# Performance work log

Measured on AMD Instinct MI355X. Metric: run time of the kernel, lower is better.

Reference implementation:

```python
import jax, jax.numpy as jnp
import numpy as np

N, T = 32, 1500
ENC_DIM, DEC_DIM = 1024, 1024
ATT_DIM, ATT_HEAD = 512, 4
HA = ATT_DIM * ATT_HEAD


def setup_inputs() -> dict:
    key = jax.random.key(0)
    ks = jax.random.split(key, 12)
    enc_pad = jax.random.normal(ks[0], (N, T, ENC_DIM), dtype=jnp.float32)
    enc_len = jax.random.randint(ks[1], (N,), T // 2, T + 1)
    enc_len = enc_len.at[0].set(T)  # ensure max == T (original code assumes mask width == T)
    dec_prev = jax.random.normal(ks[2], (N, DEC_DIM), dtype=jnp.float32)
    ali_prev = jnp.zeros((N, T), dtype=jnp.float32)  # unused by forward
    s = 0.02
    W_enc = jax.random.normal(ks[3], (ENC_DIM, HA), dtype=jnp.float32) * s
    b_enc = jnp.zeros((HA,), dtype=jnp.float32)
    W_key = jax.random.normal(ks[4], (ENC_DIM, HA), dtype=jnp.float32) * s
    W_dec = jax.random.normal(ks[5], (DEC_DIM, HA), dtype=jnp.float32) * s
    W_ctx = jax.random.normal(ks[6], (HA, ENC_DIM), dtype=jnp.float32) * s
    b_ctx = jnp.zeros((ENC_DIM,), dtype=jnp.float32)
    # grouped Conv1d(HA -> H, kernel=1, groups=H, bias=False): weight [H, A]
    w_conv = jax.random.normal(ks[7], (ATT_HEAD, ATT_DIM), dtype=jnp.float32) * s
    return dict(enc_pad=enc_pad, enc_len=enc_len, dec_prev=dec_prev, ali_prev=ali_prev,
                W_enc=W_enc, b_enc=b_enc, W_key=W_key, W_dec=W_dec,
                W_ctx=W_ctx, b_ctx=b_ctx, w_conv=w_conv)


def reference(enc_pad, enc_len, dec_prev, ali_prev,
              W_enc, b_enc, W_key, W_dec, W_ctx, b_ctx, w_conv):
    n, t, _ = enc_pad.shape
    H, A = ATT_HEAD, ATT_DIM
    # enc_part: N x H x T x A
    enc_part = (enc_pad @ W_enc + b_enc).reshape(n, t, H, A).transpose(0, 2, 1, 3)
    # key_part: N x H x A x T
    key_part = (enc_pad @ W_key).reshape(n, t, H, A).transpose(0, 2, 3, 1)
    # dec_part: N x H x A
    dec_part = (dec_prev @ W_dec).reshape(n, H, A)
    # additive score: tanh(key + dec), grouped 1x1 conv scorer -> N x H x T
    sum_part = jnp.tanh(key_part + dec_part[:, :, :, None])
    e = jnp.einsum('nhat,ha->nht', sum_part, w_conv)
    # padding mask: True where t >= enc_len
    pad_mask = jnp.arange(t)[None, :] >= enc_len[:, None]  # N x T
    e = jnp.where(pad_mask[:, None, :], -jnp.inf, e)
    ali = jax.nn.softmax(e, axis=-1)  # N x H x T
    # weighted sum over time, then context projection
    ctx = jnp.einsum('nht,nhta->nha', ali, enc_part).reshape(n, H * A)
    ctx = ctx @ W_ctx + b_ctx  # N x D_enc
    return ali, ctx
```

## Files before the change

### kernel.cpp

```cpp
#include <hip/hip_runtime.h>
#include <hip/hip_bf16.h>


#define N_B   32
#define T_S   1500
#define ENC_D 1024
#define HA_D  2048
#define A_D   512
#define H_N   4
#define MROWS 48000

typedef short s8v  __attribute__((ext_vector_type(8)));
typedef float f32x4 __attribute__((ext_vector_type(4)));

__device__ __forceinline__ unsigned short f2bf(float f) {
    unsigned u = __float_as_uint(f);
    unsigned r = (u + 0x7FFFu + ((u >> 16) & 1u)) >> 16;
    return (unsigned short)r;
}
__device__ __forceinline__ float bf2f(unsigned short b) {
    return __uint_as_float(((unsigned)b) << 16);
}
__device__ __forceinline__ float fast_tanh(float x) {
    float e2 = __expf(2.0f * x);
    return 1.0f - __fdividef(2.0f, e2 + 1.0f);
}
__device__ __forceinline__ void gload_lds16(const void* g, void* l) {
    __builtin_amdgcn_global_load_lds(
        (const unsigned int __attribute__((address_space(1)))*)g,
        (unsigned int __attribute__((address_space(3)))*)l, 16, 0, 0);
}

__device__ __forceinline__ void skinny_body(
    int bid, const float* __restrict__ X, const float* __restrict__ W,
    const float* __restrict__ bias, float* __restrict__ Y,
    int Ncols, int ct_mask, int ct_shift, int xA, int xB, float* xT ) {
    const int tid = threadIdx.x;
    const int ct = bid & ct_mask, ks = bid >> ct_shift;
    const int c0 = ct << 8, k0 = ks << 6;
    const int hsel = c0 >> 9;
    {
        const int n = tid >> 3, kk0 = (tid & 7) << 3;
        const float* xr = X + (size_t)n * xA + hsel * xB + k0 + kk0;
        float4 v0 = *(const float4*)xr;
        float4 v1 = *(const float4*)(xr + 4);
        xT[(kk0 + 0) * 36 + n] = v0.x;
        xT[(kk0 + 1) * 36 + n] = v0.y;
        xT[(kk0 + 2) * 36 + n] = v0.z;
        xT[(kk0 + 3) * 36 + n] = v0.w;
        xT[(kk0 + 4) * 36 + n] = v1.x;
        xT[(kk0 + 5) * 36 + n] = v1.y;
        xT[(kk0 + 6) * 36 + n] = v1.z;
        xT[(kk0 + 7) * 36 + n] = v1.w;
    }
    __syncthreads();
    const int w = tid >> 6, lane = tid & 63;
    f32x4 acc[8];
    if (bias != nullptr && ks == 0) {
        f32x4 bv = *(const f32x4*)&bias[c0 + (lane << 2)];
#pragma unroll
        for (int j = 0; j < 8; ++j) acc[j] = bv;
    } else {
#pragma unroll
        for (int j = 0; j < 8; ++j) { f32x4 z = {0.f, 0.f, 0.f, 0.f}; acc[j] = z; }
    }
    const float* Wp = W + (size_t)k0 * Ncols + c0 + (lane << 2);
#pragma unroll 4
    for (int kk = 0; kk < 64; ++kk) {
        f32x4 wf = *(const f32x4*)(Wp + (size_t)kk * Ncols);
        f32x4 xlo = *(const f32x4*)&xT[kk * 36 + w * 8];
        f32x4 xhi = *(const f32x4*)&xT[kk * 36 + w * 8 + 4];
#pragma unroll
        for (int j = 0; j < 4; ++j) {
            acc[j]     += xlo[j] * wf;
            acc[4 + j] += xhi[j] * wf;
        }
    }
#pragma unroll
    for (int j = 0; j < 8; ++j) {
        float* yp = Y + (size_t)(w * 8 + j) * Ncols + c0 + (lane << 2);
#pragma unroll
        for (int i = 0; i < 4; ++i) atomicAdd(yp + i, acc[j][i]);
    }
}

__global__ __launch_bounds__(256) void skinny_k(
    const float* __restrict__ X, const float* __restrict__ W,
    const float* __restrict__ bias, float* __restrict__ Y,
    int Ncols, int ct_mask, int ct_shift, int xA, int xB) {
    __shared__ float xT[64 * 36];
    skinny_body(blockIdx.x, X, W, bias, Y, Ncols, ct_mask, ct_shift, xA, xB, xT);
}

__global__ __launch_bounds__(256) void prep_k(
    const float* __restrict__ enc_pad, const float* __restrict__ Wk,
    const float* __restrict__ dec_prev, const float* __restrict__ W_dec,
    unsigned short* __restrict__ Xb, unsigned short* __restrict__ Wt,
    float* __restrict__ dp) {
    __shared__ float shmem[64 * 65];
    const int b = blockIdx.x;
    const int tid = threadIdx.x;
    if (b < 128) {
        skinny_body(b, dec_prev, W_dec, nullptr, dp, HA_D, 7, 3, 1024, 0, shmem);
    } else if (b < 640) {
        float (*ld)[65] = (float(*)[65])shmem;
        const int bb = b - 128;
        const int tx = tid & 63, ty = tid >> 6;
        const int c0 = (bb & 31) * 64, d0 = (bb >> 5) * 64;
#pragma unroll
        for (int j = 0; j < 16; ++j)
            ld[ty + 4 * j][tx] = Wk[(size_t)(d0 + ty + 4 * j) * HA_D + c0 + tx];
        __syncthreads();
#pragma unroll
        for (int j = 0; j < 16; ++j)
            Wt[(size_t)(c0 + ty + 4 * j) * ENC_D + d0 + tx] = f2bf(ld[tx][ty + 4 * j]);
    } else {
        const float4* in = (const float4*)enc_pad;
        ushort4* out = (ushort4*)Xb;
        for (int i = (b - 640) * 256 + tid; i < 12288000; i += 3000 * 256) {
            float4 v = in[i];
            ushort4 o;
            o.x = f2bf(v.x); o.y = f2bf(v.y); o.z = f2bf(v.z); o.w = f2bf(v.w);
            out[i] = o;
        }
    }
}

__global__ __launch_bounds__(512) void fused_score_k(
    const unsigned short* __restrict__ Xb, const unsigned short* __restrict__ Wt,
    const float* __restrict__ dec, const float* __restrict__ wconv,
    const int* __restrict__ enc_len, float* __restrict__ e_out) {
    __shared__ unsigned short As[128 * 64];
    __shared__ unsigned short Bs[256 * 64];
    __shared__ float e_s[128];

    const int tid = threadIdx.x;
    const int lane = tid & 63, wid = tid >> 6;
    const int wr = wid >> 2, wc = wid & 3;
    const int l15 = lane & 15, lhi = lane >> 4;

    int orig = blockIdx.x;
    int wgid = (orig & 7) * 375 + (orig >> 3);
    const int mtile = wgid >> 3, nt = wgid & 7;
    const int r0 = mtile * 128;
    const int bcol0 = nt * 256;
    const int h = nt >> 1;

    {
        int n0 = (int)((unsigned)r0 / 1500u);
        int t0 = r0 - n0 * 1500;
        if (t0 + 127 < 1500 && t0 >= enc_len[n0]) return;
    }

    if (tid < 128) e_s[tid] = 0.f;

    const unsigned short* aSrc[2]; int aDst[2];
#pragma unroll
    for (int ld = 0; ld < 2; ++ld) {
        int li = ld * 512 + tid, rowL = li >> 3, c16 = li & 7;
        aSrc[ld] = Xb + (size_t)(r0 + rowL) * ENC_D + ((c16 ^ (rowL & 7)) << 3);
        aDst[ld] = li * 8;
    }
    const unsigned short* bSrc[4]; int bDst[4];
#pragma unroll
    for (int ld = 0; ld < 4; ++ld) {
        int li = ld * 512 + tid, colL = li >> 3, c16 = li & 7;
        bSrc[ld] = Wt + (size_t)(bcol0 + colL) * ENC_D + ((c16 ^ (colL & 7)) << 3);
        bDst[ld] = li * 8;
    }

    const int cA0 = (lhi * 8) ^ ((l15 & 7) << 3);
    const int cA1 = (32 + lhi * 8) ^ ((l15 & 7) << 3);
    const int arow = wr * 64 + l15;
    const int bcol = wc * 64 + l15;

    f32x4 acc[4][4];
#pragma unroll
    for (int m = 0; m < 4; ++m)
#pragma unroll
        for (int n2 = 0; n2 < 4; ++n2) {
            f32x4 z = {0.f, 0.f, 0.f, 0.f};
            acc[m][n2] = z;
        }

    for (int ks = 0; ks < 16; ++ks) {
        const int kb = ks << 6;
#pragma unroll
        for (int ld = 0; ld < 2; ++ld) gload_lds16(aSrc[ld] + kb, As + aDst[ld]);
#pragma unroll
        for (int ld = 0; ld < 4; ++ld) gload_lds16(bSrc[ld] + kb, Bs + bDst[ld]);
        __syncthreads();
#pragma unroll
        for (int kk = 0; kk < 2; ++kk) {
            const int cc = kk ? cA1 : cA0;
            s8v af[4], bv[4];
#pragma unroll
            for (int m = 0; m < 4; ++m)
                af[m] = *(const s8v*)&As[(arow + m * 16) * 64 + cc];
#pragma unroll
            for (int n2 = 0; n2 < 4; ++n2)
                bv[n2] = *(const s8v*)&Bs[(bcol + n2 * 16) * 64 + cc];
#pragma unroll
            for (int m = 0; m < 4; ++m)
#pragma unroll
                for (int n2 = 0; n2 < 4; ++n2)
                    acc[m][n2] = __builtin_amdgcn_mfma_f32_16x16x32_bf16(af[m], bv[n2], acc[m][n2], 0, 0, 0);
        }
        __syncthreads();
    }

    float wv[4];
#pragma unroll
    for (int n2 = 0; n2 < 4; ++n2)
        wv[n2] = wconv[bcol0 + wc * 64 + n2 * 16 + l15];
#pragma unroll
    for (int m = 0; m < 4; ++m) {
#pragma unroll
        for (int rg = 0; rg < 4; ++rg) {
            int row_l = wr * 64 + m * 16 + lhi * 4 + rg;
            int grow = r0 + row_l;
            int nn = (int)((unsigned)grow / 1500u);
            const float* dsl = dec + (size_t)nn * HA_D + bcol0 + wc * 64 + l15;
            float s = 0.f;
#pragma unroll
            for (int n2 = 0; n2 < 4; ++n2) {
                float v = acc[m][n2][rg] + dsl[n2 * 16];
                s += wv[n2] * fast_tanh(v);
            }
            s += __shfl_xor(s, 1); s += __shfl_xor(s, 2);
            s += __shfl_xor(s, 4); s += __shfl_xor(s, 8);
            if (l15 == 0) atomicAdd(&e_s[row_l], s);
        }
    }
    __syncthreads();
    if (tid < 128) {
        int grow = r0 + tid;
        int nn = grow / 1500, tt = grow - nn * 1500;
        atomicAdd(&e_out[(size_t)(nn * H_N + h) * T_S + tt], e_s[tid]);
    }
}

__global__ void softmax_k(const float* __restrict__ e, const int* __restrict__ enc_len,
                          float* __restrict__ ali, float* __restrict__ ctx_zero) {
    const int tid = threadIdx.x, lane = tid & 63, wid = tid >> 6;
    ctx_zero[blockIdx.x * 256 + tid] = 0.f;
    const int n = blockIdx.x >> 2;
    const int len = enc_len[n];
    const float* row = e + (size_t)blockIdx.x * T_S;
    float* orow = ali + (size_t)blockIdx.x * T_S;
    __shared__ float red[4];
    float p[6];
    float mx = -__builtin_inff();
#pragma unroll
    for (int i = 0; i < 6; ++i) {
        int t = tid + i * 256;
        float v = -__builtin_inff();
        if (t < T_S && t < len) v = row[t];
        p[i] = v;
        mx = fmaxf(mx, v);
    }
#pragma unroll
    for (int o = 32; o; o >>= 1) mx = fmaxf(mx, __shfl_xor(mx, o));
    if (lane == 0) red[wid] = mx;
    __syncthreads();
    mx = fmaxf(fmaxf(red[0], red[1]), fmaxf(red[2], red[3]));
    __syncthreads();
    float sum = 0.f;
#pragma unroll
    for (int i = 0; i < 6; ++i) {
        float qv = (p[i] == -__builtin_inff()) ? 0.f : __expf(p[i] - mx);
        p[i] = qv;
        sum += qv;
    }
#pragma unroll
    for (int o = 32; o; o >>= 1) sum += __shfl_xor(sum, o);
    if (lane == 0) red[wid] = sum;
    __syncthreads();
    sum = red[0] + red[1] + red[2] + red[3];
    float inv = 1.0f / sum;
#pragma unroll
    for (int i = 0; i < 6; ++i) {
        int t = tid + i * 256;
        if (t < T_S) orow[t] = p[i] * inv;
    }
}

__global__ __launch_bounds__(256) void wenc_k(const unsigned short* __restrict__ Xb,
                                              const float* __restrict__ ali,
                                              const int* __restrict__ enc_len,
                                              float* __restrict__ wenc) {
    const int tid = threadIdx.x;
    const int n = blockIdx.x & 31, tq = blockIdx.x >> 5;
    const int t0 = tq * 94;
    const int tcnt = (t0 + 94 <= T_S) ? 94 : (T_S - t0);
    if (t0 >= enc_len[n]) return;
    __shared__ float alis[4][94];
    for (int i = tid; i < 376; i += 256) {
        int hh = i / 94, tt = i - hh * 94;
        if (tt < tcnt) alis[hh][tt] = ali[(size_t)(n * H_N + hh) * T_S + t0 + tt];
    }
    __syncthreads();
    const int d0 = tid * 4;
    float a[4][4] = {};
    const unsigned short* xp = Xb + (size_t)(n * T_S + t0) * ENC_D + d0;
#pragma unroll 4
    for (int t = 0; t < tcnt; ++t) {
        ushort4 xv = *(const ushort4*)&xp[(size_t)t * ENC_D];
        float x0 = bf2f(xv.x), x1 = bf2f(xv.y), x2 = bf2f(xv.z), x3 = bf2f(xv.w);
#pragma unroll
        for (int hh = 0; hh < 4; ++hh) {
            float al = alis[hh][t];
            a[hh][0] = fmaf(al, x0, a[hh][0]);
            a[hh][1] = fmaf(al, x1, a[hh][1]);
            a[hh][2] = fmaf(al, x2, a[hh][2]);
            a[hh][3] = fmaf(al, x3, a[hh][3]);
        }
    }
#pragma unroll
    for (int hh = 0; hh < 4; ++hh)
#pragma unroll
        for (int j = 0; j < 4; ++j)
            atomicAdd(&wenc[(size_t)(n * H_N + hh) * ENC_D + d0 + j], a[hh][j]);
}

extern "C" void kernel_launch(void* const* d_in, const int* in_sizes, int n_in,
                              void* d_out, int out_size, void* d_ws, size_t ws_size,
                              hipStream_t stream) {
    const float* enc_pad  = (const float*)d_in[0];
    const int*   enc_len  = (const int*)d_in[1];
    const float* dec_prev = (const float*)d_in[2];
    const float* W_enc    = (const float*)d_in[4];
    const float* b_enc    = (const float*)d_in[5];
    const float* W_key    = (const float*)d_in[6];
    const float* W_dec    = (const float*)d_in[7];
    const float* W_ctx    = (const float*)d_in[8];
    const float* b_ctx    = (const float*)d_in[9];
    const float* w_conv   = (const float*)d_in[10];

    char* ws = (char*)d_ws;
    unsigned short* Xb = (unsigned short*)ws;
    unsigned short* Wt = (unsigned short*)(ws + 98304000);
    float* dp   = (float*)(ws + 102498304);
    float* e    = (float*)(ws + 102760448);
    float* wenc = (float*)(ws + 103528448);
    float* cpre = (float*)(ws + 104052736);

    float* ali = (float*)d_out;
    float* ctx = ((float*)d_out) + 192000;

    hipMemsetAsync(ws + 102498304, 0, 1816576, stream);
    prep_k<<<3640, 256, 0, stream>>>(enc_pad, W_key, dec_prev, W_dec, Xb, Wt, dp);
    fused_score_k<<<3000, 512, 0, stream>>>(Xb, Wt, dp, w_conv, enc_len, e);
    softmax_k<<<128, 256, 0, stream>>>(e, enc_len, ali, ctx);
    wenc_k<<<512, 256, 0, stream>>>(Xb, ali, enc_len, wenc);
    skinny_k<<<128, 256, 0, stream>>>(wenc, W_enc, b_enc, cpre, HA_D, 7, 3, 4096, 1024);
    skinny_k<<<128, 256, 0, stream>>>(cpre, W_ctx, b_ctx, ctx, ENC_D, 3, 2, 2048, 0);
}
```

Measured before the change: 405.5 us.

## Fuse softmax into weighted-sum kernel and skip bf16 conversion of padded rows

The enc_pad-to-bf16 conversion in prep_k is now tiled per (batch, 16-timestep chunk) and skips chunks beyond enc_len, so padded timesteps are neither read nor converted. Softmax and the alignment-weighted sum are merged into one launch: each weighted-sum block recomputes per-head max and normalizer from the raw scores and builds its own probabilities, while extra blocks write the ali output and zero ctx. This removes a kernel launch and the dependency on ali being written first, at the cost of redundant max/sum reductions in every block. The unconverted Xb rows for padded timesteps are left holding stale data, which relies on downstream consumers masking them.

```diff
diff --git a/kernel.cpp b/kernel.cpp
--- a/kernel.cpp
+++ b/kernel.cpp
@@ -95,6 +95,7 @@
 __global__ __launch_bounds__(256) void prep_k(
     const float* __restrict__ enc_pad, const float* __restrict__ Wk,
     const float* __restrict__ dec_prev, const float* __restrict__ W_dec,
+    const int* __restrict__ enc_len,
     unsigned short* __restrict__ Xb, unsigned short* __restrict__ Wt,
     float* __restrict__ dp) {
     __shared__ float shmem[64 * 65];
@@ -115,13 +116,22 @@
         for (int j = 0; j < 16; ++j)
             Wt[(size_t)(c0 + ty + 4 * j) * ENC_D + d0 + tx] = f2bf(ld[tx][ty + 4 * j]);
     } else {
-        const float4* in = (const float4*)enc_pad;
-        ushort4* out = (ushort4*)Xb;
-        for (int i = (b - 640) * 256 + tid; i < 12288000; i += 3000 * 256) {
-            float4 v = in[i];
-            ushort4 o;
-            o.x = f2bf(v.x); o.y = f2bf(v.y); o.z = f2bf(v.z); o.w = f2bf(v.w);
-            out[i] = o;
+        const int cb = b - 640;
+        const int n = cb / 94, tch = cb - n * 94;
+        const int t0 = tch * 16;
+        if (t0 >= enc_len[n]) return;
+        const int rmax = (1500 - t0 < 16) ? (1500 - t0) : 16;
+        const float4* in = (const float4*)enc_pad + ((size_t)n * 1500 + t0) * 256;
+        ushort4* out = (ushort4*)Xb + ((size_t)n * 1500 + t0) * 256;
+#pragma unroll
+        for (int it = 0; it < 16; ++it) {
+            int j = it * 256 + tid;
+            if ((j >> 8) < rmax) {
+                float4 v = in[j];
+                ushort4 o;
+                o.x = f2bf(v.x); o.y = f2bf(v.y); o.z = f2bf(v.z); o.w = f2bf(v.w);
+                out[j] = o;
+            }
         }
     }
 }
@@ -240,87 +250,118 @@
     }
 }
 
-__global__ void softmax_k(const float* __restrict__ e, const int* __restrict__ enc_len,
-                          float* __restrict__ ali, float* __restrict__ ctx_zero) {
-    const int tid = threadIdx.x, lane = tid & 63, wid = tid >> 6;
-    ctx_zero[blockIdx.x * 256 + tid] = 0.f;
-    const int n = blockIdx.x >> 2;
-    const int len = enc_len[n];
-    const float* row = e + (size_t)blockIdx.x * T_S;
-    float* orow = ali + (size_t)blockIdx.x * T_S;
+__global__ __launch_bounds__(256) void sm_wenc_k(
+    const unsigned short* __restrict__ Xb, const float* __restrict__ e,
+    const int* __restrict__ enc_len, float* __restrict__ ali,
+    float* __restrict__ ctx_zero, float* __restrict__ wenc) {
+    const int b = blockIdx.x, tid = threadIdx.x;
+    const int lane = tid & 63, wv = tid >> 6;
+    __shared__ float mzs[4][2];
+    __shared__ float ps[4][94];
     __shared__ float red[4];
-    float p[6];
-    float mx = -__builtin_inff();
-#pragma unroll
-    for (int i = 0; i < 6; ++i) {
-        int t = tid + i * 256;
-        float v = -__builtin_inff();
-        if (t < T_S && t < len) v = row[t];
-        p[i] = v;
-        mx = fmaxf(mx, v);
-    }
-#pragma unroll
-    for (int o = 32; o; o >>= 1) mx = fmaxf(mx, __shfl_xor(mx, o));
-    if (lane == 0) red[wid] = mx;
-    __syncthreads();
-    mx = fmaxf(fmaxf(red[0], red[1]), fmaxf(red[2], red[3]));
-    __syncthreads();
-    float sum = 0.f;
-#pragma unroll
-    for (int i = 0; i < 6; ++i) {
-        float qv = (p[i] == -__builtin_inff()) ? 0.f : __expf(p[i] - mx);
-        p[i] = qv;
-        sum += qv;
-    }
-#pragma unroll
-    for (int o = 32; o; o >>= 1) sum += __shfl_xor(sum, o);
-    if (lane == 0) red[wid] = sum;
-    __syncthreads();
-    sum = red[0] + red[1] + red[2] + red[3];
-    float inv = 1.0f / sum;
-#pragma unroll
-    for (int i = 0; i < 6; ++i) {
-        int t = tid + i * 256;
-        if (t < T_S) orow[t] = p[i] * inv;
-    }
-}
-
-__global__ __launch_bounds__(256) void wenc_k(const unsigned short* __restrict__ Xb,
-                                              const float* __restrict__ ali,
-                                              const int* __restrict__ enc_len,
-                                              float* __restrict__ wenc) {
-    const int tid = threadIdx.x;
-    const int n = blockIdx.x & 31, tq = blockIdx.x >> 5;
-    const int t0 = tq * 94;
-    const int tcnt = (t0 + 94 <= T_S) ? 94 : (T_S - t0);
-    if (t0 >= enc_len[n]) return;
-    __shared__ float alis[4][94];
-    for (int i = tid; i < 376; i += 256) {
-        int hh = i / 94, tt = i - hh * 94;
-        if (tt < tcnt) alis[hh][tt] = ali[(size_t)(n * H_N + hh) * T_S + t0 + tt];
-    }
-    __syncthreads();
-    const int d0 = tid * 4;
-    float a[4][4] = {};
-    const unsigned short* xp = Xb + (size_t)(n * T_S + t0) * ENC_D + d0;
+    if (b < 512) {
+        const int n = b >> 4, tq = b & 15;
+        const int len = enc_len[n];
+        const int t0 = tq * 94;
+        if (t0 >= len) return;
+        const int tcnt = (t0 + 94 <= T_S) ? 94 : (T_S - t0);
+        {
+            const float* erow = e + (size_t)(n * H_N + wv) * T_S;
+            float ev[24];
+            float mx = -__builtin_inff();
+#pragma unroll
+            for (int i = 0; i < 24; ++i) {
+                int t = lane + i * 64;
+                float v = (t < len) ? erow[t] : -__builtin_inff();
+                ev[i] = v;
+                mx = fmaxf(mx, v);
+            }
+#pragma unroll
+            for (int o = 32; o; o >>= 1) mx = fmaxf(mx, __shfl_xor(mx, o));
+            float Z = 0.f;
+#pragma unroll
+            for (int i = 0; i < 24; ++i) Z += __expf(ev[i] - mx);
+#pragma unroll
+            for (int o = 32; o; o >>= 1) Z += __shfl_xor(Z, o);
+            if (lane == 0) { mzs[wv][0] = mx; mzs[wv][1] = 1.0f / Z; }
+        }
+        __syncthreads();
+#pragma unroll
+        for (int i = 0; i < 2; ++i) {
+            int idx = tid + i * 256;
+            if (idx < 376) {
+                int hh = idx / 94, tt = idx - hh * 94;
+                int t = t0 + tt;
+                float v = 0.f;
+                if (t < len)
+                    v = __expf(e[(size_t)(n * H_N + hh) * T_S + t] - mzs[hh][0]) * mzs[hh][1];
+                ps[hh][tt] = v;
+            }
+        }
+        __syncthreads();
+        const int d0 = tid * 4;
+        float a[4][4] = {};
+        const unsigned short* xp = Xb + (size_t)(n * T_S + t0) * ENC_D + d0;
 #pragma unroll 4
-    for (int t = 0; t < tcnt; ++t) {
-        ushort4 xv = *(const ushort4*)&xp[(size_t)t * ENC_D];
-        float x0 = bf2f(xv.x), x1 = bf2f(xv.y), x2 = bf2f(xv.z), x3 = bf2f(xv.w);
-#pragma unroll
-        for (int hh = 0; hh < 4; ++hh) {
-            float al = alis[hh][t];
-            a[hh][0] = fmaf(al, x0, a[hh][0]);
-            a[hh][1] = fmaf(al, x1, a[hh][1]);
-            a[hh][2] = fmaf(al, x2, a[hh][2]);
-            a[hh][3] = fmaf(al, x3, a[hh][3]);
-        }
-    }
-#pragma unroll
-    for (int hh = 0; hh < 4; ++hh)
-#pragma unroll
-        for (int j = 0; j < 4; ++j)
-            atomicAdd(&wenc[(size_t)(n * H_N + hh) * ENC_D + d0 + j], a[hh][j]);
+        for (int t = 0; t < tcnt; ++t) {
+            ushort4 xv = *(const ushort4*)&xp[(size_t)t * ENC_D];
+            float x0 = bf2f(xv.x), x1 = bf2f(xv.y), x2 = bf2f(xv.z), x3 = bf2f(xv.w);
+#pragma unroll
+            for (int hh = 0; hh < 4; ++hh) {
+                float al = ps[hh][t];
+                a[hh][0] = fmaf(al, x0, a[hh][0]);
+                a[hh][1] = fmaf(al, x1, a[hh][1]);
+                a[hh][2] = fmaf(al, x2, a[hh][2]);
+                a[hh][3] = fmaf(al, x3, a[hh][3]);
+            }
+        }
+#pragma unroll
+        for (int hh = 0; hh < 4; ++hh)
+#pragma unroll
+            for (int j = 0; j < 4; ++j)
+                atomicAdd(&wenc[(size_t)(n * H_N + hh) * ENC_D + d0 + j], a[hh][j]);
+    } else {
+        const int bb = b - 512;
+        ctx_zero[bb * 256 + tid] = 0.f;
+        const int n = bb >> 2;
+        const int len = enc_len[n];
+        const float* row = e + (size_t)bb * T_S;
+        float* orow = ali + (size_t)bb * T_S;
+        float p[6];
+        float mx = -__builtin_inff();
+#pragma unroll
+        for (int i = 0; i < 6; ++i) {
+            int t = tid + i * 256;
+            float v = -__builtin_inff();
+            if (t < T_S && t < len) v = row[t];
+            p[i] = v;
+            mx = fmaxf(mx, v);
+        }
+#pragma unroll
+        for (int o = 32; o; o >>= 1) mx = fmaxf(mx, __shfl_xor(mx, o));
+        if (lane == 0) red[wv] = mx;
+        __syncthreads();
+        mx = fmaxf(fmaxf(red[0], red[1]), fmaxf(red[2], red[3]));
+        __syncthreads();
+        float sum = 0.f;
+#pragma unroll
+        for (int i = 0; i < 6; ++i) {
+            float qv = (p[i] == -__builtin_inff()) ? 0.f : __expf(p[i] - mx);
+            p[i] = qv;
+            sum += qv;
+        }
+#pragma unroll
+        for (int o = 32; o; o >>= 1) sum += __shfl_xor(sum, o);
+        if (lane == 0) red[wv] = sum;
+        __syncthreads();
+        sum = red[0] + red[1] + red[2] + red[3];
+        float inv = 1.0f / sum;
+#pragma unroll
+        for (int i = 0; i < 6; ++i) {
+            int t = tid + i * 256;
+            if (t < T_S) orow[t] = p[i] * inv;
+        }
+    }
 }
 
 extern "C" void kernel_launch(void* const* d_in, const int* in_sizes, int n_in,
@@ -349,10 +390,9 @@
     float* ctx = ((float*)d_out) + 192000;
 
     hipMemsetAsync(ws + 102498304, 0, 1816576, stream);
-    prep_k<<<3640, 256, 0, stream>>>(enc_pad, W_key, dec_prev, W_dec, Xb, Wt, dp);
+    prep_k<<<3648, 256, 0, stream>>>(enc_pad, W_key, dec_prev, W_dec, enc_len, Xb, Wt, dp);
     fused_score_k<<<3000, 512, 0, stream>>>(Xb, Wt, dp, w_conv, enc_len, e);
-    softmax_k<<<128, 256, 0, stream>>>(e, enc_len, ali, ctx);
-    wenc_k<<<512, 256, 0, stream>>>(Xb, ali, enc_len, wenc);
+    sm_wenc_k<<<640, 256, 0, stream>>>(Xb, e, enc_len, ali, ctx, wenc);
     skinny_k<<<128, 256, 0, stream>>>(wenc, W_enc, b_enc, cpre, HA_D, 7, 3, 4096, 1024);
     skinny_k<<<128, 256, 0, stream>>>(cpre, W_ctx, b_ctx, ctx, ENC_D, 3, 2, 2048, 0);
 }
```

New measurement: 362.6 us, median of 3. 1.12x faster.
